# Performance work log

Measured on AMD Instinct MI355X. Metric: run time of the kernel, lower is better.

Reference implementation:

```python
import jax, jax.numpy as jnp
import numpy as np

N = 100000          # nodes
E = 1600000         # edges (avg degree 16)
NUM_NODES = 100000  # embedding vocab
EMB = 128
HID = 64
G = 256             # graphs in the batch


def setup_inputs() -> dict:
    key = jax.random.key(0)
    ks = jax.random.split(key, 14)
    x_ids = jax.random.randint(ks[0], (N,), 0, NUM_NODES)
    edge_index = jax.random.randint(ks[1], (2, E), 0, N)
    batch = jnp.sort(jax.random.randint(ks[2], (N,), 0, G))
    s = 0.05
    emb = jax.random.normal(ks[3], (NUM_NODES, EMB), jnp.float32) * s
    W1 = jax.random.normal(ks[4], (EMB, HID), jnp.float32) * s
    b1 = jnp.zeros((HID,), jnp.float32)
    W2 = jax.random.normal(ks[5], (HID, HID), jnp.float32) * s
    b2 = jnp.zeros((HID,), jnp.float32)
    W3 = jax.random.normal(ks[6], (HID, HID), jnp.float32) * s
    b3 = jnp.zeros((HID,), jnp.float32)
    Wf1 = jax.random.normal(ks[7], (HID, HID), jnp.float32) * s
    bf1 = jnp.zeros((HID,), jnp.float32)
    Wf2 = jax.random.normal(ks[8], (HID, 1), jnp.float32) * s
    bf2 = jnp.zeros((1,), jnp.float32)
    return dict(x_ids=x_ids, edge_index=edge_index, batch=batch, emb=emb,
                W1=W1, b1=b1, W2=W2, b2=b2, W3=W3, b3=b3,
                Wf1=Wf1, bf1=bf1, Wf2=Wf2, bf2=bf2)


def gcn_conv(x, W, b, src, dst, num_nodes):
    # PyG GCNConv: x' = D^{-1/2} (A + I) D^{-1/2} (x W) + b
    xw = x @ W  # [N, out]
    ones = jnp.ones(src.shape[0], x.dtype)
    deg = jax.ops.segment_sum(ones, dst, num_segments=num_nodes) + 1.0  # self-loop
    dinv = jax.lax.rsqrt(deg)
    coef = dinv[src] * dinv[dst]  # per-edge norm
    agg = jax.ops.segment_sum(xw[src] * coef[:, None], dst, num_segments=num_nodes)
    agg = agg + xw * (dinv * dinv)[:, None]  # self-loop message
    return agg + b


def reference(x_ids, edge_index, batch, emb, W1, b1, W2, b2, W3, b3, Wf1, bf1, Wf2, bf2):
    src, dst = edge_index[0], edge_index[1]
    x = emb[x_ids]                                   # [N, EMB]
    x = jax.nn.relu(gcn_conv(x, W1, b1, src, dst, N))
    x = jax.nn.relu(gcn_conv(x, W2, b2, src, dst, N))
    x = jax.nn.relu(gcn_conv(x, W3, b3, src, dst, N))
    # global mean pool per graph
    counts = jax.ops.segment_sum(jnp.ones(N, x.dtype), batch, num_segments=G)
    pooled = jax.ops.segment_sum(x, batch, num_segments=G) / jnp.maximum(counts, 1.0)[:, None]
    h = jax.nn.relu(pooled @ Wf1 + bf1)
    out = (h @ Wf2 + bf2).squeeze(-1)                # [G]
    return jax.nn.sigmoid(out)
```

## Files before the change

kernel.cpp:

```cpp
#include <hip/hip_runtime.h>
#include <hip/hip_bf16.h>
#include <hip/hip_fp8.h>


typedef unsigned char u8;
typedef unsigned short u16;
typedef unsigned int u32;

#define FSCALE 256.0f
#define SINV (1.0f / 256.0f)
#define S2 65536.0f

__device__ __forceinline__ float fp8d(u32 b) {
#if __has_builtin(__builtin_amdgcn_cvt_f32_fp8)
  return __builtin_amdgcn_cvt_f32_fp8((int)b, 0);
#else
  __hip_fp8_e4m3 t; t.__x = (__hip_fp8_storage_t)b; return (float)t;
#endif
}
__device__ __forceinline__ u32 fp8e1(float f) {
#if __has_builtin(__builtin_amdgcn_cvt_pk_fp8_f32)
  return (u32)__builtin_amdgcn_cvt_pk_fp8_f32(f, 0.f, 0, false) & 0xffu;
#else
  __hip_fp8_e4m3 t(f); return (u32)t.__x;
#endif
}
__device__ __forceinline__ u32 fp8e4(float f0, float f1, float f2, float f3) {
#if __has_builtin(__builtin_amdgcn_cvt_pk_fp8_f32)
  int r = 0;
  r = __builtin_amdgcn_cvt_pk_fp8_f32(f0, f1, r, false);
  r = __builtin_amdgcn_cvt_pk_fp8_f32(f2, f3, r, true);
  return (u32)r;
#else
  __hip_fp8_e4m3 a(f0), b(f1), c(f2), d(f3);
  return (u32)a.__x | ((u32)b.__x << 8) | ((u32)c.__x << 16) | ((u32)d.__x << 24);
#endif
}

__global__ __launch_bounds__(256) void k_init(int* __restrict__ cnt8, int n8,
                                              u8* __restrict__ rowA, u8* __restrict__ rowB) {
  int i = blockIdx.x * blockDim.x + threadIdx.x;
  int stride = gridDim.x * blockDim.x;
  for (; i < n8; i += stride) cnt8[i] = 0;
  if (blockIdx.x == 0 && threadIdx.x < 64) {
    rowA[threadIdx.x] = 0;
    rowB[threadIdx.x] = 0;
  }
}

__global__ __launch_bounds__(256) void k_count_rank(const int* __restrict__ dst, int* __restrict__ cnt8,
                                                    int* __restrict__ rank, int e_count, int n) {
  int e = blockIdx.x * blockDim.x + threadIdx.x;
  if (e < e_count) {
    int p = blockIdx.x & 7;
    rank[e] = atomicAdd(&cnt8[p * n + dst[e]], 1);
  }
}

__global__ __launch_bounds__(256) void k_scan1(const int* __restrict__ cnt8, int n, int* __restrict__ bsum) {
  __shared__ int s[256];
  int b = blockIdx.x, t = threadIdx.x;
  int base = b * 1024;
  int sum = 0;
  #pragma unroll
  for (int i = 0; i < 4; ++i) {
    int idx = base + t + i * 256;
    if (idx < n) {
      int c = 0;
      #pragma unroll
      for (int q = 0; q < 8; ++q) c += cnt8[q * n + idx];
      sum += (c + 7) & ~7;
    }
  }
  s[t] = sum; __syncthreads();
  for (int off = 128; off > 0; off >>= 1) {
    if (t < off) s[t] += s[t + off];
    __syncthreads();
  }
  if (t == 0) bsum[b] = s[0];
}

__global__ __launch_bounds__(128) void k_scan2(int* __restrict__ bsum, int nb, int* __restrict__ total_out) {
  __shared__ int sh[128];
  int t = threadIdx.x;
  sh[t] = (t < nb) ? bsum[t] : 0;
  __syncthreads();
  for (int off = 1; off < 128; off <<= 1) {
    int x = sh[t];
    int y = (t >= off) ? sh[t - off] : 0;
    __syncthreads();
    sh[t] = x + y;
    __syncthreads();
  }
  if (t < nb) bsum[t] = (t == 0) ? 0 : sh[t - 1];
  if (t == 0) *total_out = sh[127];
}

__global__ __launch_bounds__(256) void k_scan3(int* __restrict__ cnt8, int n,
                                               const int* __restrict__ bsum_ex, int* __restrict__ offsets,
                                               float* __restrict__ dsc, u32* __restrict__ csr) {
  __shared__ int sh[256];
  int b = blockIdx.x, t = threadIdx.x;
  int base = b * 1024 + t * 4;
  int cq[4][8];
  int c[4], v[4];
  #pragma unroll
  for (int i = 0; i < 4; ++i) {
    c[i] = 0;
    #pragma unroll
    for (int q = 0; q < 8; ++q) {
      int x = (base + i < n) ? cnt8[q * n + base + i] : 0;
      cq[i][q] = x;
      c[i] += x;
    }
    v[i] = (c[i] + 7) & ~7;
    if (base + i < n) dsc[base + i] = rsqrtf((float)c[i] + 1.0f) * SINV;
  }
  sh[t] = v[0] + v[1] + v[2] + v[3];
  __syncthreads();
  for (int off = 1; off < 256; off <<= 1) {
    int x = sh[t];
    int y = (t >= off) ? sh[t - off] : 0;
    __syncthreads();
    sh[t] = x + y;
    __syncthreads();
  }
  int run = bsum_ex[b] + ((t == 0) ? 0 : sh[t - 1]);
  #pragma unroll
  for (int i = 0; i < 4; ++i) {
    if (base + i < n) {
      offsets[base + i] = run;
      int pb = run;
      #pragma unroll
      for (int q = 0; q < 8; ++q) {
        cnt8[q * n + base + i] = pb;
        pb += cq[i][q];
      }
      for (int j = run + c[i]; j < run + v[i]; ++j) csr[j] = (u32)n;
      run += v[i];
    }
  }
  if (b == 0 && t == 0) dsc[n] = 0.f;
}

__global__ __launch_bounds__(256, 4) void k_mm1_scatter(
    const int* __restrict__ ids, const float* __restrict__ emb,
    const float* __restrict__ W1, u8* __restrict__ out, int n, int mmb,
    const int* __restrict__ src, const int* __restrict__ dst,
    const int* __restrict__ rank, const int* __restrict__ pbase,
    const float* __restrict__ dsc, u32* __restrict__ csr, int e_count) {
  if ((int)blockIdx.x >= mmb) {
    int eb = blockIdx.x - mmb;
    int e = eb * 256 + threadIdx.x;
    if (e < e_count) {
      int p = eb & 7;
      int d = dst[e];
      int pos = pbase[p * n + d] + rank[e];
      __builtin_nontemporal_store((u32)src[e], &csr[pos]);
    }
    return;
  }

  const int lane = threadIdx.x & 63;
  const int w = threadIdx.x >> 6;
  const int r = blockIdx.x * 256 + w * 64 + lane;
  const int rc = (r < n) ? r : (n - 1);
  const int rid = ids[rc];
  const float zs = dsc[rc] * S2;
  const float4* __restrict__ xrow = reinterpret_cast<const float4*>(emb + (size_t)rid * 128);

  float acc[64];
  #pragma unroll
  for (int j = 0; j < 64; ++j) acc[j] = 0.f;

  #pragma unroll 1
  for (int s = 0; s < 4; ++s) {
    float4 xb[8];
    #pragma unroll
    for (int i = 0; i < 8; ++i) xb[i] = xrow[s * 8 + i];
    const float* __restrict__ wbase = W1 + (size_t)(s * 32) * 64;
    #pragma unroll
    for (int i = 0; i < 8; ++i) {
      const float* __restrict__ w0 = wbase + (i * 4) * 64;
      #pragma unroll
      for (int j = 0; j < 64; ++j) {
        acc[j] = fmaf(xb[i].x, w0[j], acc[j]);
        acc[j] = fmaf(xb[i].y, w0[64 + j], acc[j]);
        acc[j] = fmaf(xb[i].z, w0[128 + j], acc[j]);
        acc[j] = fmaf(xb[i].w, w0[192 + j], acc[j]);
      }
    }
  }

  if (r < n) {
    u8* op = out + (size_t)r * 64;
    #pragma unroll
    for (int q = 0; q < 4; ++q) {
      uint4 pk;
      pk.x = fp8e4(acc[q * 16 + 0] * zs, acc[q * 16 + 1] * zs,
                   acc[q * 16 + 2] * zs, acc[q * 16 + 3] * zs);
      pk.y = fp8e4(acc[q * 16 + 4] * zs, acc[q * 16 + 5] * zs,
                   acc[q * 16 + 6] * zs, acc[q * 16 + 7] * zs);
      pk.z = fp8e4(acc[q * 16 + 8] * zs, acc[q * 16 + 9] * zs,
                   acc[q * 16 + 10] * zs, acc[q * 16 + 11] * zs);
      pk.w = fp8e4(acc[q * 16 + 12] * zs, acc[q * 16 + 13] * zs,
                   acc[q * 16 + 14] * zs, acc[q * 16 + 15] * zs);
      *reinterpret_cast<uint4*>(op + q * 16) = pk;
    }
  }
}


#define G8(dstreg, OFF)                                                      \
  _Pragma("unroll")                                                          \
  for (int t_ = 0; t_ < 8; ++t_) {                                           \
    int sb_ = __builtin_amdgcn_readlane((int)ce, (OFF) + t_);                \
    dstreg[t_] = (u32)z[(size_t)sb_ * 64 + lane];                            \
  }

#define C8(srcreg, OFF)                                                      \
  {                                                                          \
    float tmp_ = 0.f;                                                        \
    _Pragma("unroll")                                                        \
    for (int t_ = 0; t_ < 8; ++t_) tmp_ += fp8d(srcreg[t_]);                 \
    const int ep_ = e + (OFF);                                               \
    if (ep_ < b1) acc0 = fmaf(tmp_, d0, acc0);                               \
    else if (ep_ < b2) acc1 = fmaf(tmp_, d1, acc1);                          \
    else if (ep_ < b3) acc2 = fmaf(tmp_, d2, acc2);                          \
    else acc3 = fmaf(tmp_, d3, acc3);                                        \
  }

template <bool FINAL>
__global__ __launch_bounds__(256, 4) void k_agg(const u8* __restrict__ z, const u32* __restrict__ csr,
                                                const int* __restrict__ offs, const float* __restrict__ dsc,
                                                const float* __restrict__ bias, const float* __restrict__ Wn,
                                                u8* __restrict__ out, int n) {
  const int lane = threadIdx.x & 63;
  const int w = threadIdx.x >> 6;
  const int ngroups = (n + 3) >> 2;
  const int grp = blockIdx.x * 4 + w;
  if (grp >= ngroups) return;
  const float bl = bias[lane];

  const int v0 = grp * 4;
  const int c1 = (v0 + 1 < n) ? v0 + 1 : n;
  const int c2 = (v0 + 2 < n) ? v0 + 2 : n;
  const int c3 = (v0 + 3 < n) ? v0 + 3 : n;
  const int b0 = offs[v0], b1 = offs[c1], b2 = offs[c2], b3 = offs[c3];
  const int b4 = offs[(v0 + 4 < n) ? v0 + 4 : n];

  const float d0 = dsc[v0];
  const float d1 = dsc[(c1 < n) ? c1 : v0];
  const float d2 = dsc[(c2 < n) ? c2 : v0];
  const float d3 = dsc[(c3 < n) ? c3 : v0];
  float acc0 = fmaf(fp8d(z[(size_t)v0 * 64 + lane]), d0, bl);
  float acc1 = (c1 < n) ? fmaf(fp8d(z[(size_t)c1 * 64 + lane]), d1, bl) : 0.f;
  float acc2 = (c2 < n) ? fmaf(fp8d(z[(size_t)c2 * 64 + lane]), d2, bl) : 0.f;
  float acc3 = (c3 < n) ? fmaf(fp8d(z[(size_t)c3 * 64 + lane]), d3, bl) : 0.f;

  int e = b0;
  while (e < b4) {
    u32 ce = (u32)n;
    if (lane < b4 - e) ce = csr[e + lane];
    u32 gA[8], gB[8], gC[8], gD[8];
    G8(gA, 0)
    G8(gB, 8)
    G8(gC, 16)
    G8(gD, 24)
    C8(gA, 0)
    G8(gA, 32)
    C8(gB, 8)
    G8(gB, 40)
    C8(gC, 16)
    G8(gC, 48)
    C8(gD, 24)
    G8(gD, 56)
    C8(gA, 32)
    C8(gB, 40)
    C8(gC, 48)
    C8(gD, 56)
    e += 64;
  }

  float h0 = fmaxf(acc0, 0.f), h1 = fmaxf(acc1, 0.f);
  float h2 = fmaxf(acc2, 0.f), h3 = fmaxf(acc3, 0.f);
  if constexpr (FINAL) {
    out[(size_t)v0 * 64 + lane] = (u8)fp8e1(h0 * FSCALE);
    if (c1 < n) out[(size_t)c1 * 64 + lane] = (u8)fp8e1(h1 * FSCALE);
    if (c2 < n) out[(size_t)c2 * 64 + lane] = (u8)fp8e1(h2 * FSCALE);
    if (c3 < n) out[(size_t)c3 * 64 + lane] = (u8)fp8e1(h3 * FSCALE);
  } else {
    const int hb0 = __float_as_int(h0), hb1 = __float_as_int(h1);
    const int hb2 = __float_as_int(h2), hb3 = __float_as_int(h3);
    float o0 = 0.f, o1 = 0.f, o2 = 0.f, o3 = 0.f;
    #pragma unroll
    for (int k = 0; k < 64; ++k) {
      float wk = Wn[k * 64 + lane];
      o0 = fmaf(__int_as_float(__builtin_amdgcn_readlane(hb0, k)), wk, o0);
      o1 = fmaf(__int_as_float(__builtin_amdgcn_readlane(hb1, k)), wk, o1);
      o2 = fmaf(__int_as_float(__builtin_amdgcn_readlane(hb2, k)), wk, o2);
      o3 = fmaf(__int_as_float(__builtin_amdgcn_readlane(hb3, k)), wk, o3);
    }
    out[(size_t)v0 * 64 + lane] = (u8)fp8e1(o0 * d0 * S2);
    if (c1 < n) out[(size_t)c1 * 64 + lane] = (u8)fp8e1(o1 * d1 * S2);
    if (c2 < n) out[(size_t)c2 * 64 + lane] = (u8)fp8e1(o2 * d2 * S2);
    if (c3 < n) out[(size_t)c3 * 64 + lane] = (u8)fp8e1(o3 * d3 * S2);
  }
}

__global__ __launch_bounds__(256) void k_pool(const u8* __restrict__ x, const int* __restrict__ batch, int n,
                                              const float* __restrict__ Wf1, const float* __restrict__ bf1,
                                              const float* __restrict__ Wf2, const float* __restrict__ bf2,
                                              float* __restrict__ out) {
  int g = blockIdx.x;
  int tid = threadIdx.x, lane = tid & 63, w = tid >> 6;
  int a = 0, b = n;
  while (a < b) { int m = (a + b) >> 1; if (batch[m] < g) a = m + 1; else b = m; }
  int lo = a;
  b = n;
  while (a < b) { int m = (a + b) >> 1; if (batch[m] < g + 1) a = m + 1; else b = m; }
  int hi = a;

  float acc = 0.f;
  for (int r = lo + w; r < hi; r += 4) acc += fp8d(x[(size_t)r * 64 + lane]);
  __shared__ float red[4][64];
  __shared__ float mean[64];
  red[w][lane] = acc;
  __syncthreads();
  if (w == 0) {
    float s = red[0][lane] + red[1][lane] + red[2][lane] + red[3][lane];
    mean[lane] = s / (fmaxf((float)(hi - lo), 1.0f) * FSCALE);
  }
  __syncthreads();
  if (w == 0) {
    float h = bf1[lane];
    #pragma unroll
    for (int k = 0; k < 64; ++k) h = fmaf(mean[k], Wf1[k * 64 + lane], h);
    h = fmaxf(h, 0.f);
    float vv = h * Wf2[lane];
    for (int off = 32; off > 0; off >>= 1) vv += __shfl_down(vv, off, 64);
    if (lane == 0) out[g] = 1.0f / (1.0f + expf(-(vv + bf2[0])));
  }
}

static inline char* align256(char* p) {
  return (char*)(((uintptr_t)p + 255) & ~(uintptr_t)255);
}

extern "C" void kernel_launch(void* const* d_in, const int* in_sizes, int n_in,
                              void* d_out, int out_size, void* d_ws, size_t ws_size,
                              hipStream_t stream) {
  const int*   x_ids = (const int*)d_in[0];
  const int*   edge  = (const int*)d_in[1];
  const int*   batch = (const int*)d_in[2];
  const float* emb   = (const float*)d_in[3];
  const float* W1    = (const float*)d_in[4];
  const float* b1    = (const float*)d_in[5];
  const float* W2    = (const float*)d_in[6];
  const float* b2    = (const float*)d_in[7];
  const float* W3    = (const float*)d_in[8];
  const float* b3    = (const float*)d_in[9];
  const float* Wf1   = (const float*)d_in[10];
  const float* bf1   = (const float*)d_in[11];
  const float* Wf2   = (const float*)d_in[12];
  const float* bf2   = (const float*)d_in[13];
  float* out = (float*)d_out;

  const int N = in_sizes[0];
  const int E = in_sizes[1] / 2;
  const int G = out_size;
  const int* e_src = edge;
  const int* e_dst = edge + E;

  const size_t EPAD = (size_t)E + 8 * (size_t)(N + 1) + 128;

  char* p = (char*)d_ws;
  u8*    bufA = (u8*)p;               p = align256(p + (size_t)(N + 1) * 64);
  u8*    bufB = (u8*)p;               p = align256(p + (size_t)(N + 1) * 64);
  u32*   csr  = (u32*)p;              p = align256(p + EPAD * 4);
  int*   rank = (int*)p;              p = align256(p + (size_t)E * 4);
  float* dsc  = (float*)p;            p = align256(p + (size_t)(N + 1) * 4);
  int*   cnt8 = (int*)p;              p = align256(p + (size_t)8 * N * 4);
  int*   offs = (int*)p;              p = align256(p + (size_t)(N + 1) * 4);
  int*   bsum = (int*)p;              p = align256(p + (size_t)1024 * 4);
  (void)ws_size; (void)n_in;

  const int nb_scan = (N + 1023) / 1024;
  dim3 blk(256);

  k_init<<<dim3(512), blk, 0, stream>>>(cnt8, 8 * N, bufA + (size_t)N * 64, bufB + (size_t)N * 64);
  k_count_rank<<<dim3((E + 255) / 256), blk, 0, stream>>>(e_dst, cnt8, rank, E, N);
  k_scan1<<<dim3(nb_scan), blk, 0, stream>>>(cnt8, N, bsum);
  k_scan2<<<dim3(1), dim3(128), 0, stream>>>(bsum, nb_scan, offs + N);
  k_scan3<<<dim3(nb_scan), blk, 0, stream>>>(cnt8, N, bsum, offs, dsc, csr);

  const int mmb = (N + 255) / 256;
  const int scb = (E + 255) / 256;
  k_mm1_scatter<<<dim3(mmb + scb), blk, 0, stream>>>(
      x_ids, emb, W1, bufA, N, mmb,
      e_src, e_dst, rank, cnt8, dsc, csr, E);

  const int ngroups = (N + 3) / 4;
  const int agg_grid = (ngroups + 3) / 4;
  k_agg<false><<<dim3(agg_grid), blk, 0, stream>>>(bufA, csr, offs, dsc, b1, W2, bufB, N);
  k_agg<false><<<dim3(agg_grid), blk, 0, stream>>>(bufB, csr, offs, dsc, b2, W3, bufA, N);
  k_agg<true><<<dim3(agg_grid), blk, 0, stream>>>(bufA, csr, offs, dsc, b3, nullptr, bufB, N);

  k_pool<<<dim3(G), blk, 0, stream>>>(bufB, batch, N, Wf1, bf1, Wf2, bf2, out);
}
```

Measured before the change: 356.9 us.

## Gather fp8 rows as dwords across 16-lane groups and pad CSR to four

Restructures the GCN aggregation so each wave gathers four neighbour rows at once. Each 16-lane quarter loads a 32-bit word holding four fp8 features, replacing one byte per lane per neighbour. Partial sums are kept per feature quad and reduced across quarters with shuffles at the end. Per-node CSR padding drops from multiples of 8 to multiples of 4, and blocks past the edge count are skipped, cutting wasted padded gathers. The cost is extra shuffle reduction work and more divergent branching in the unrolled gather chain.

```diff
diff --git a/kernel.cpp b/kernel.cpp
--- a/kernel.cpp
+++ b/kernel.cpp
@@ -15,9 +15,14 @@
 #if __has_builtin(__builtin_amdgcn_cvt_f32_fp8)
   return __builtin_amdgcn_cvt_f32_fp8((int)b, 0);
 #else
-  __hip_fp8_e4m3 t; t.__x = (__hip_fp8_storage_t)b; return (float)t;
+  __hip_fp8_e4m3 t; t.__x = (__hip_fp8_storage_t)(b & 0xffu); return (float)t;
 #endif
 }
+#if __has_builtin(__builtin_amdgcn_cvt_f32_fp8)
+#define FP8DSEL(dw, s) __builtin_amdgcn_cvt_f32_fp8((int)(dw), (s))
+#else
+#define FP8DSEL(dw, s) fp8d(((dw) >> (8 * (s))) & 0xffu)
+#endif
 __device__ __forceinline__ u32 fp8e1(float f) {
 #if __has_builtin(__builtin_amdgcn_cvt_pk_fp8_f32)
   return (u32)__builtin_amdgcn_cvt_pk_fp8_f32(f, 0.f, 0, false) & 0xffu;
@@ -69,7 +74,7 @@
       int c = 0;
       #pragma unroll
       for (int q = 0; q < 8; ++q) c += cnt8[q * n + idx];
-      sum += (c + 7) & ~7;
+      sum += (c + 3) & ~3;
     }
   }
   s[t] = sum; __syncthreads();
@@ -113,7 +118,7 @@
       cq[i][q] = x;
       c[i] += x;
     }
-    v[i] = (c[i] + 7) & ~7;
+    v[i] = (c[i] + 3) & ~3;
     if (base + i < n) dsc[base + i] = rsqrtf((float)c[i] + 1.0f) * SINV;
   }
   sh[t] = v[0] + v[1] + v[2] + v[3];
@@ -211,23 +216,40 @@
 }
 
 
-#define G8(dstreg, OFF)                                                      \
-  _Pragma("unroll")                                                          \
-  for (int t_ = 0; t_ < 8; ++t_) {                                           \
-    int sb_ = __builtin_amdgcn_readlane((int)ce, (OFF) + t_);                \
-    dstreg[t_] = (u32)z[(size_t)sb_ * 64 + lane];                            \
-  }
-
-#define C8(srcreg, OFF)                                                      \
+#define G4(dstreg, CE, B)                                                    \
   {                                                                          \
-    float tmp_ = 0.f;                                                        \
+    int sb_ = __shfl((int)(CE), (B) * 4 + s4, 64);                           \
+    dstreg = z32[(size_t)sb_ * 16 + q];                                      \
+  }
+
+#define C4(srcreg, B)                                                        \
+  {                                                                          \
+    float f0_ = FP8DSEL(srcreg, 0);                                          \
+    float f1_ = FP8DSEL(srcreg, 1);                                          \
+    float f2_ = FP8DSEL(srcreg, 2);                                          \
+    float f3_ = FP8DSEL(srcreg, 3);                                          \
+    const int ep_ = e + (B) * 4;                                             \
+    if (ep_ < b1)      { pa0[0] += f0_; pa0[1] += f1_; pa0[2] += f2_; pa0[3] += f3_; } \
+    else if (ep_ < b2) { pa1[0] += f0_; pa1[1] += f1_; pa1[2] += f2_; pa1[3] += f3_; } \
+    else if (ep_ < b3) { pa2[0] += f0_; pa2[1] += f1_; pa2[2] += f2_; pa2[3] += f3_; } \
+    else               { pa3[0] += f0_; pa3[1] += f1_; pa3[2] += f2_; pa3[3] += f3_; } \
+  }
+
+#define NSUM(pa, OUTV)                                                       \
+  {                                                                          \
     _Pragma("unroll")                                                        \
-    for (int t_ = 0; t_ < 8; ++t_) tmp_ += fp8d(srcreg[t_]);                 \
-    const int ep_ = e + (OFF);                                               \
-    if (ep_ < b1) acc0 = fmaf(tmp_, d0, acc0);                               \
-    else if (ep_ < b2) acc1 = fmaf(tmp_, d1, acc1);                          \
-    else if (ep_ < b3) acc2 = fmaf(tmp_, d2, acc2);                          \
-    else acc3 = fmaf(tmp_, d3, acc3);                                        \
+    for (int r_ = 0; r_ < 4; ++r_) {                                         \
+      pa[r_] += __shfl_xor(pa[r_], 16, 64);                                  \
+      pa[r_] += __shfl_xor(pa[r_], 32, 64);                                  \
+    }                                                                        \
+    int ls_ = lane >> 2;                                                     \
+    float t0_ = __shfl(pa[0], ls_, 64);                                      \
+    float t1_ = __shfl(pa[1], ls_, 64);                                      \
+    float t2_ = __shfl(pa[2], ls_, 64);                                      \
+    float t3_ = __shfl(pa[3], ls_, 64);                                      \
+    float s01_ = (lane & 1) ? t1_ : t0_;                                     \
+    float s23_ = (lane & 1) ? t3_ : t2_;                                     \
+    OUTV = (lane & 2) ? s23_ : s01_;                                         \
   }
 
 template <bool FINAL>
@@ -237,6 +259,9 @@
                                                 u8* __restrict__ out, int n) {
   const int lane = threadIdx.x & 63;
   const int w = threadIdx.x >> 6;
+  const int s4 = lane >> 4;
+  const int q = lane & 15;
+  const u32* __restrict__ z32 = reinterpret_cast<const u32*>(z);
   const int ngroups = (n + 3) >> 2;
   const int grp = blockIdx.x * 4 + w;
   if (grp >= ngroups) return;
@@ -253,37 +278,60 @@
   const float d1 = dsc[(c1 < n) ? c1 : v0];
   const float d2 = dsc[(c2 < n) ? c2 : v0];
   const float d3 = dsc[(c3 < n) ? c3 : v0];
-  float acc0 = fmaf(fp8d(z[(size_t)v0 * 64 + lane]), d0, bl);
-  float acc1 = (c1 < n) ? fmaf(fp8d(z[(size_t)c1 * 64 + lane]), d1, bl) : 0.f;
-  float acc2 = (c2 < n) ? fmaf(fp8d(z[(size_t)c2 * 64 + lane]), d2, bl) : 0.f;
-  float acc3 = (c3 < n) ? fmaf(fp8d(z[(size_t)c3 * 64 + lane]), d3, bl) : 0.f;
+
+  float pa0[4] = {0.f, 0.f, 0.f, 0.f};
+  float pa1[4] = {0.f, 0.f, 0.f, 0.f};
+  float pa2[4] = {0.f, 0.f, 0.f, 0.f};
+  float pa3[4] = {0.f, 0.f, 0.f, 0.f};
 
   int e = b0;
   while (e < b4) {
+    int cnt = b4 - e;
+    cnt = (cnt < 64) ? cnt : 64;
+    const int nb = cnt >> 2;
     u32 ce = (u32)n;
-    if (lane < b4 - e) ce = csr[e + lane];
-    u32 gA[8], gB[8], gC[8], gD[8];
-    G8(gA, 0)
-    G8(gB, 8)
-    G8(gC, 16)
-    G8(gD, 24)
-    C8(gA, 0)
-    G8(gA, 32)
-    C8(gB, 8)
-    G8(gB, 40)
-    C8(gC, 16)
-    G8(gC, 48)
-    C8(gD, 24)
-    G8(gD, 56)
-    C8(gA, 32)
-    C8(gB, 40)
-    C8(gC, 48)
-    C8(gD, 56)
-    e += 64;
-  }
-
-  float h0 = fmaxf(acc0, 0.f), h1 = fmaxf(acc1, 0.f);
-  float h2 = fmaxf(acc2, 0.f), h3 = fmaxf(acc3, 0.f);
+    if (lane < cnt) ce = csr[e + lane];
+
+    u32 g0, g1, g2, g3, g4, g5, g6, g7;
+    G4(g0, ce, 0)
+    if (nb > 1) G4(g1, ce, 1)
+    if (nb > 2) G4(g2, ce, 2)
+    if (nb > 3) G4(g3, ce, 3)
+    if (nb > 4) G4(g4, ce, 4)
+    if (nb > 5) G4(g5, ce, 5)
+    if (nb > 6) G4(g6, ce, 6)
+    if (nb > 7) G4(g7, ce, 7)
+    { C4(g0, 0)               if (nb > 8)  G4(g0, ce, 8)  }
+    if (nb > 1)  { C4(g1, 1)  if (nb > 9)  G4(g1, ce, 9)  }
+    if (nb > 2)  { C4(g2, 2)  if (nb > 10) G4(g2, ce, 10) }
+    if (nb > 3)  { C4(g3, 3)  if (nb > 11) G4(g3, ce, 11) }
+    if (nb > 4)  { C4(g4, 4)  if (nb > 12) G4(g4, ce, 12) }
+    if (nb > 5)  { C4(g5, 5)  if (nb > 13) G4(g5, ce, 13) }
+    if (nb > 6)  { C4(g6, 6)  if (nb > 14) G4(g6, ce, 14) }
+    if (nb > 7)  { C4(g7, 7)  if (nb > 15) G4(g7, ce, 15) }
+    if (nb > 8)  { C4(g0, 8)  }
+    if (nb > 9)  { C4(g1, 9)  }
+    if (nb > 10) { C4(g2, 10) }
+    if (nb > 11) { C4(g3, 11) }
+    if (nb > 12) { C4(g4, 12) }
+    if (nb > 13) { C4(g5, 13) }
+    if (nb > 14) { C4(g6, 14) }
+    if (nb > 15) { C4(g7, 15) }
+    e += cnt;
+  }
+
+  float ns0, ns1, ns2, ns3;
+  NSUM(pa0, ns0)
+  NSUM(pa1, ns1)
+  NSUM(pa2, ns2)
+  NSUM(pa3, ns3)
+
+  float h0 = fmaxf(fmaf(ns0 + fp8d(z[(size_t)v0 * 64 + lane]), d0, bl), 0.f);
+  float h1 = 0.f, h2 = 0.f, h3 = 0.f;
+  if (c1 < n) h1 = fmaxf(fmaf(ns1 + fp8d(z[(size_t)c1 * 64 + lane]), d1, bl), 0.f);
+  if (c2 < n) h2 = fmaxf(fmaf(ns2 + fp8d(z[(size_t)c2 * 64 + lane]), d2, bl), 0.f);
+  if (c3 < n) h3 = fmaxf(fmaf(ns3 + fp8d(z[(size_t)c3 * 64 + lane]), d3, bl), 0.f);
+
   if constexpr (FINAL) {
     out[(size_t)v0 * 64 + lane] = (u8)fp8e1(h0 * FSCALE);
     if (c1 < n) out[(size_t)c1 * 64 + lane] = (u8)fp8e1(h1 * FSCALE);
@@ -372,7 +420,7 @@
   const int* e_src = edge;
   const int* e_dst = edge + E;
 
-  const size_t EPAD = (size_t)E + 8 * (size_t)(N + 1) + 128;
+  const size_t EPAD = (size_t)E + 4 * (size_t)(N + 1) + 256;
 
   char* p = (char*)d_ws;
   u8*    bufA = (u8*)p;               p = align256(p + (size_t)(N + 1) * 64);
```

New measurement: 341.6 us. 4.3% less time.
